# Kernel tuning notes

Measured on AMD Instinct MI355X. Metric: run time of the kernel, lower is better.

The kernel has to match this reference:

```python
import jax, jax.numpy as jnp
import numpy as np

N = 30000      # nodes
E = 480000     # edges (before self loops)
NFEAT = 128
H = 16         # heads
C = 32         # per-head channels = nhid
NCLASS = 10
G = 64         # graphs in batch
ATT_SLOPE = 0.2   # GATv2Conv negative_slope default
ACT_SLOPE = 0.01  # F.leaky_relu default


def setup_inputs() -> dict:
    key = jax.random.key(0)
    ks = jax.random.split(key, 16)
    def glorot(k, shape):
        fan = sum(shape[:2]) if len(shape) > 1 else shape[0]
        return jax.random.normal(k, shape, jnp.float32) * (2.0 / fan) ** 0.5
    inp = {
        "x": jax.random.normal(ks[0], (N, NFEAT), jnp.float32),
        # layer 1: lin_l / lin_r map NFEAT -> H*C, attention vector att [H, C]
        "Wl1": glorot(ks[1], (NFEAT, H * C)), "bl1": jnp.zeros((H * C,), jnp.float32),
        "Wr1": glorot(ks[2], (NFEAT, H * C)), "br1": jnp.zeros((H * C,), jnp.float32),
        "att1": glorot(ks[3], (H, C)), "b1": jnp.zeros((C,), jnp.float32),
        # layer 2: nhid(=C) -> H*C
        "Wl2": glorot(ks[4], (C, H * C)), "bl2": jnp.zeros((H * C,), jnp.float32),
        "Wr2": glorot(ks[5], (C, H * C)), "br2": jnp.zeros((H * C,), jnp.float32),
        "att2": glorot(ks[6], (H, C)), "b2": jnp.zeros((C,), jnp.float32),
        # classifier nhid -> nclass
        "Wc": glorot(ks[7], (C, NCLASS)), "bc": jnp.zeros((NCLASS,), jnp.float32),
        "edge_index": jax.random.randint(ks[8], (2, E), 0, N, jnp.int32),
        "batch": jnp.sort(jax.random.randint(ks[9], (N,), 0, G, jnp.int32)),
    }
    return inp


def _gatv2_layer(x, Wl, bl, Wr, br, att, b, src, dst, n):
    # GATv2Conv, concat=False (mean over heads), eval mode (no dropout)
    xl = (x @ Wl + bl).reshape(n, H, C)   # messages (x_j)
    xr = (x @ Wr + br).reshape(n, H, C)   # query side (x_i)
    e = jax.nn.leaky_relu(xl[src] + xr[dst], ATT_SLOPE)      # [E', H, C]
    score = jnp.einsum('ehc,hc->eh', e, att)                 # [E', H]
    # segment softmax over incoming edges of each dst node
    m = jax.ops.segment_max(score, dst, num_segments=n)
    ex = jnp.exp(score - m[dst])
    denom = jax.ops.segment_sum(ex, dst, num_segments=n)
    alpha = ex / denom[dst]                                  # [E', H]
    out = jax.ops.segment_sum(alpha[:, :, None] * xl[src], dst, num_segments=n)
    return out.mean(axis=1) + b                              # [n, C]


def reference(x, Wl1, bl1, Wr1, br1, att1, b1, Wl2, bl2, Wr2, br2, att2, b2, Wc, bc, edge_index, batch):
    # add self loops (PyG GATv2Conv default add_self_loops=True)
    loop = jnp.arange(N, dtype=edge_index.dtype)
    src = jnp.concatenate([edge_index[0], loop])
    dst = jnp.concatenate([edge_index[1], loop])

    h = jax.nn.leaky_relu(_gatv2_layer(x, Wl1, bl1, Wr1, br1, att1, b1, src, dst, N), ACT_SLOPE)
    h = jax.nn.leaky_relu(_gatv2_layer(h, Wl2, bl2, Wr2, br2, att2, b2, src, dst, N), ACT_SLOPE)
    # dropout is identity in eval mode
    # global mean pool over graphs
    summed = jax.ops.segment_sum(h, batch, num_segments=G)               # [G, C]
    counts = jax.ops.segment_sum(jnp.ones((N,), h.dtype), batch, num_segments=G)
    pooled = summed / jnp.maximum(counts, 1.0)[:, None]
    logits = pooled @ Wc + bc
    return logits / 1.0  # temperature = 1.0
```

## Files before the change

kernel.cpp:

```cpp
#include <hip/hip_runtime.h>
#include <float.h>

#define NNODES 30000
#define NEDGES 480000
#define NFEATK 128
#define NH 16
#define NC 32
#define HC 512
#define NCLASSES 10
#define NG 64
#define CAP 96

using half2v = __attribute__((ext_vector_type(2))) _Float16;
using half4 = __attribute__((ext_vector_type(4))) _Float16;
using half8 = __attribute__((ext_vector_type(8))) _Float16;
using f32x4 = __attribute__((ext_vector_type(4))) float;

__global__ void prep0_kernel(const float* __restrict__ Wl1, const float* __restrict__ Wr1,
                             _Float16* __restrict__ Wlt1, _Float16* __restrict__ Wrt1,
                             const float* __restrict__ Wl2, const float* __restrict__ Wr2,
                             _Float16* __restrict__ Wlt2, _Float16* __restrict__ Wrt2,
                             int* __restrict__ cnt, unsigned short* __restrict__ csr) {
    int gtid = blockIdx.x * blockDim.x + threadIdx.x;
    int gstride = gridDim.x * blockDim.x;
    for (int i = gtid; i < 2 * 512 * NFEATK; i += gstride) {
        int sel = i >= 512 * NFEATK;
        int idx = i - sel * 512 * NFEATK;
        const float* W = sel ? Wr1 : Wl1;
        _Float16* Wt = sel ? Wrt1 : Wlt1;
        int n = idx & 511, k = idx >> 9;
        Wt[n * NFEATK + k] = (_Float16)W[idx];
    }
    for (int i = gtid; i < 2 * 512 * NC; i += gstride) {
        int sel = i >= 512 * NC;
        int idx = i - sel * 512 * NC;
        const float* W = sel ? Wr2 : Wl2;
        _Float16* Wt = sel ? Wrt2 : Wlt2;
        int n = idx & 511, k = idx >> 9;
        Wt[n * NC + k] = (_Float16)W[idx];
    }
    for (int i = gtid; i < NNODES; i += gstride) {
        cnt[i] = 1;
        csr[i * CAP] = (unsigned short)i;
    }
}

__global__ void scatter_kernel(const int* __restrict__ src, const int* __restrict__ dst,
                               int* __restrict__ cnt, unsigned short* __restrict__ csr) {
    int e = blockIdx.x * blockDim.x + threadIdx.x;
    if (e >= NEDGES) return;
    int s = src[e], d = dst[e];
    int pos = atomicAdd(&cnt[d], 1);
    csr[d * CAP + pos] = (unsigned short)s;
}

template <int K, typename AT>
__launch_bounds__(256)
__global__ void dual_gemm_kernel(const AT* __restrict__ A,
                                 const _Float16* __restrict__ Wlt, const _Float16* __restrict__ Wrt,
                                 const float* __restrict__ bl, const float* __restrict__ br,
                                 _Float16* __restrict__ Yl, _Float16* __restrict__ Yr) {
    constexpr int KS = (K > 64) ? 64 : K;
    constexpr int KcS = KS / 8;
    constexpr int AH = 64 * KS;
    constexpr int BH = 128 * KS;
    constexpr int YSH = 64 * 136;
    constexpr int SMEMH = (AH + 2 * BH > YSH) ? (AH + 2 * BH) : YSH;
    __shared__ __align__(16) _Float16 smem[SMEMH];
    _Float16* as = smem;
    _Float16* bsl = smem + AH;
    _Float16* bsr = smem + AH + BH;

    int tid = threadIdx.x;
    int nbase = blockIdx.x * 128;
    int mb = blockIdx.y;

    int wave = tid >> 6, lane = tid & 63;
    int quad = lane >> 4, l16 = lane & 15;
    int am = l16 & (KcS - 1);

    f32x4 accl[8], accr[8];
    #pragma unroll
    for (int f = 0; f < 8; f++) {
        accl[f] = (f32x4){0.f, 0.f, 0.f, 0.f};
        accr[f] = (f32x4){0.f, 0.f, 0.f, 0.f};
    }

    #pragma unroll
    for (int ko = 0; ko < K / KS; ++ko) {
        if (ko) __syncthreads();
        for (int c = tid; c < 64 * KcS; c += 256) {
            int row = c / KcS, k8 = c % KcS;
            int arow = mb * 64 + row; if (arow > NNODES - 1) arow = NNODES - 1;
            half8 v;
            if constexpr (sizeof(AT) == 4) {
                const float* ap = (const float*)&A[(size_t)arow * K + (ko * KcS + k8) * 8];
                float4 f0 = *(const float4*)ap;
                float4 f1 = *(const float4*)(ap + 4);
                v = half8{(_Float16)f0.x, (_Float16)f0.y, (_Float16)f0.z, (_Float16)f0.w,
                          (_Float16)f1.x, (_Float16)f1.y, (_Float16)f1.z, (_Float16)f1.w};
            } else {
                v = *(const half8*)&A[(size_t)arow * K + (ko * KcS + k8) * 8];
            }
            *(half8*)&as[(row * KcS + (k8 ^ (row & (KcS - 1)))) * 8] = v;
        }
        for (int c = tid; c < 2 * 128 * KcS; c += 256) {
            int sel = c >= 128 * KcS;
            int cc = c - sel * 128 * KcS;
            int row = cc / KcS, k8 = cc % KcS;
            const _Float16* Bt = sel ? Wrt : Wlt;
            _Float16* bs = sel ? bsr : bsl;
            half8 v = *(const half8*)&Bt[(size_t)(nbase + row) * K + (ko * KcS + k8) * 8];
            *(half8*)&bs[(row * KcS + (k8 ^ (row & (KcS - 1)))) * 8] = v;
        }
        __syncthreads();

        #pragma unroll
        for (int kk = 0; kk < KcS; kk += 4) {
            int k8 = (kk + quad) ^ am;
            half8 a = *(const half8*)&as[((wave * 16 + l16) * KcS + k8) * 8];
            #pragma unroll
            for (int f = 0; f < 8; f++) {
                half8 b = *(const half8*)&bsl[((f * 16 + l16) * KcS + k8) * 8];
                accl[f] = __builtin_amdgcn_mfma_f32_16x16x32_f16(a, b, accl[f], 0, 0, 0);
            }
            #pragma unroll
            for (int f = 0; f < 8; f++) {
                half8 b = *(const half8*)&bsr[((f * 16 + l16) * KcS + k8) * 8];
                accr[f] = __builtin_amdgcn_mfma_f32_16x16x32_f16(a, b, accr[f], 0, 0, 0);
            }
        }
    }
    __syncthreads();

    _Float16* ys = smem;
    int mtop = mb * 64;
    #pragma unroll
    for (int f = 0; f < 8; f++) {
        float bv = bl[nbase + f * 16 + l16];
        #pragma unroll
        for (int r = 0; r < 4; r++)
            ys[(wave * 16 + quad * 4 + r) * 136 + f * 16 + l16] = (_Float16)(accl[f][r] + bv);
    }
    __syncthreads();
    for (int c = tid; c < 64 * 16; c += 256) {
        int r = c >> 4, cc = (c & 15) * 8;
        int grow = mtop + r;
        if (grow < NNODES)
            *(half8*)&Yl[(size_t)grow * HC + nbase + cc] = *(half8*)&ys[r * 136 + cc];
    }
    __syncthreads();
    #pragma unroll
    for (int f = 0; f < 8; f++) {
        float bv = br[nbase + f * 16 + l16];
        #pragma unroll
        for (int r = 0; r < 4; r++)
            ys[(wave * 16 + quad * 4 + r) * 136 + f * 16 + l16] = (_Float16)(accr[f][r] + bv);
    }
    __syncthreads();
    for (int c = tid; c < 64 * 16; c += 256) {
        int r = c >> 4, cc = (c & 15) * 8;
        int grow = mtop + r;
        if (grow < NNODES)
            *(half8*)&Yr[(size_t)grow * HC + nbase + cc] = *(half8*)&ys[r * 136 + cc];
    }
}

__device__ inline half2v lrelu2(half2v e) {
    half2v s = e * half2v{(_Float16)0.2f, (_Float16)0.2f};
    return __builtin_elementwise_max(e, s);
}

#if __has_builtin(__builtin_amdgcn_fdot2)
#define FDOT2(a, b, c) __builtin_amdgcn_fdot2((a), (b), (c), false)
#else
__device__ inline float fdot2_sw(half2v a, half2v b, float c) {
    half2v p = a * b;
    return c + (float)p.x + (float)p.y;
}
#define FDOT2(a, b, c) fdot2_sw((a), (b), (c))
#endif

template <typename OUT>
__launch_bounds__(256)
__global__ void gat_edge_kernel(const _Float16* __restrict__ xlh, const _Float16* __restrict__ xrh,
                                const float* __restrict__ att, const float* __restrict__ bvec,
                                const int* __restrict__ cnt, const unsigned short* __restrict__ csr_src,
                                OUT* __restrict__ hout) {
    int wv = threadIdx.x >> 6;
    int t = threadIdx.x & 63;
    int d = blockIdx.x * 4 + wv;
    int col = t * 8;

    half8 xrq = *(const half8*)&xrh[(unsigned)d * HC + col];
    half2v xr0 = {xrq[0], xrq[1]}, xr1 = {xrq[2], xrq[3]};
    half2v xr2 = {xrq[4], xrq[5]}, xr3 = {xrq[6], xrq[7]};
    float4 atta = *(const float4*)&att[col];
    float4 attb = *(const float4*)&att[col + 4];
    half2v at0 = {(_Float16)atta.x, (_Float16)atta.y};
    half2v at1 = {(_Float16)atta.z, (_Float16)atta.w};
    half2v at2 = {(_Float16)attb.x, (_Float16)attb.y};
    half2v at3 = {(_Float16)attb.z, (_Float16)attb.w};

    int beg = d * CAP, end = beg + cnt[d];

    float l = 0.f;
    float a[8];
    #pragma unroll
    for (int c = 0; c < 8; c++) a[c] = 0.f;

    for (int i = beg; i < end; i += 8) {
        int n = end - i;
        int sx[8];
        #pragma unroll
        for (int j = 0; j < 8; j++) sx[j] = csr_src[i + (j < n ? j : 0)];
        half8 q[8];
        #pragma unroll
        for (int j = 0; j < 8; j++) q[j] = *(const half8*)&xlh[(unsigned)sx[j] * HC + col];

        float v[8];
        #pragma unroll
        for (int j = 0; j < 8; j++) {
            float vv = 0.f;
            vv = FDOT2(lrelu2(half2v{q[j][0], q[j][1]} + xr0), at0, vv);
            vv = FDOT2(lrelu2(half2v{q[j][2], q[j][3]} + xr1), at1, vv);
            vv = FDOT2(lrelu2(half2v{q[j][4], q[j][5]} + xr2), at2, vv);
            vv = FDOT2(lrelu2(half2v{q[j][6], q[j][7]} + xr3), at3, vv);
            vv += __shfl_xor(vv, 1);
            vv += __shfl_xor(vv, 2);
            v[j] = vv;
        }
        #pragma unroll
        for (int j = 0; j < 8; j++) {
            float p = (j < n) ? __expf(v[j]) : 0.f;
            l += p;
            #pragma unroll
            for (int c = 0; c < 8; c++) a[c] += p * (float)q[j][c];
        }
    }

    float inv = 1.0f / l;
    #pragma unroll
    for (int c = 0; c < 8; c++) a[c] *= inv;

    #pragma unroll
    for (int off = 4; off < 64; off <<= 1) {
        #pragma unroll
        for (int c = 0; c < 8; c++) a[c] += __shfl_xor(a[c], off);
    }

    if (t < 4) {
        #pragma unroll
        for (int c = 0; c < 8; c++) {
            float r = a[c] * (1.0f / (float)NH) + bvec[t * 8 + c];
            r = (r > 0.f) ? r : 0.01f * r;
            hout[(size_t)d * NC + t * 8 + c] = (OUT)r;
        }
    }
}

__launch_bounds__(1024)
__global__ void pool_classify_kernel(const float* __restrict__ h, const int* __restrict__ batch,
                                     const float* __restrict__ Wc, const float* __restrict__ bc,
                                     float* __restrict__ out) {
    int g = blockIdx.x;
    int lo = 0, hi = NNODES;
    while (lo < hi) { int mid = (lo + hi) >> 1; if (batch[mid] < g) lo = mid + 1; else hi = mid; }
    int start = lo;
    hi = NNODES;
    while (lo < hi) { int mid = (lo + hi) >> 1; if (batch[mid] <= g) lo = mid + 1; else hi = mid; }
    int endn = lo;
    int cntg = endn - start;

    int tid = threadIdx.x;
    int c = tid & 31, nl = tid >> 5;
    float s = 0.f;
    for (int n = start + nl; n < endn; n += 32) s += h[n * NC + c];
    __shared__ float red[1024];
    red[tid] = s;
    __syncthreads();
    if (tid < 32) {
        float t = 0.f;
        #pragma unroll
        for (int j = 0; j < 32; j++) t += red[j * 32 + tid];
        red[tid] = t / fmaxf((float)cntg, 1.0f);
    }
    __syncthreads();
    if (tid < NCLASSES) {
        float sum = bc[tid];
        #pragma unroll
        for (int cc = 0; cc < NC; cc++) sum += red[cc] * Wc[cc * NCLASSES + tid];
        out[g * NCLASSES + tid] = sum;
    }
}


extern "C" void kernel_launch(void* const* d_in, const int* in_sizes, int n_in,
                              void* d_out, int out_size, void* d_ws, size_t ws_size,
                              hipStream_t stream) {
    const float* x    = (const float*)d_in[0];
    const float* Wl1  = (const float*)d_in[1];
    const float* bl1  = (const float*)d_in[2];
    const float* Wr1  = (const float*)d_in[3];
    const float* br1  = (const float*)d_in[4];
    const float* att1 = (const float*)d_in[5];
    const float* b1   = (const float*)d_in[6];
    const float* Wl2  = (const float*)d_in[7];
    const float* bl2  = (const float*)d_in[8];
    const float* Wr2  = (const float*)d_in[9];
    const float* br2  = (const float*)d_in[10];
    const float* att2 = (const float*)d_in[11];
    const float* b2   = (const float*)d_in[12];
    const float* Wc   = (const float*)d_in[13];
    const float* bc   = (const float*)d_in[14];
    const int* ei     = (const int*)d_in[15];
    const int* batch  = (const int*)d_in[16];
    float* out = (float*)d_out;

    const int* srcp = ei;
    const int* dstp = ei + NEDGES;

    char* ws = (char*)d_ws;
    size_t off = 0;
    auto alloc = [&](size_t bytes) -> void* {
        void* p = ws + off;
        off += (bytes + 255) & ~(size_t)255;
        return p;
    };
    _Float16* xlh  = (_Float16*)alloc(sizeof(_Float16) * (size_t)NNODES * HC);
    _Float16* xrh  = (_Float16*)alloc(sizeof(_Float16) * (size_t)NNODES * HC);
    _Float16* h1   = (_Float16*)alloc(sizeof(_Float16) * (size_t)NNODES * NC);
    float* h2      = (float*)alloc(sizeof(float) * (size_t)NNODES * NC);
    _Float16* Wlt1 = (_Float16*)alloc(sizeof(_Float16) * 512 * NFEATK);
    _Float16* Wrt1 = (_Float16*)alloc(sizeof(_Float16) * 512 * NFEATK);
    _Float16* Wlt2 = (_Float16*)alloc(sizeof(_Float16) * 512 * NC);
    _Float16* Wrt2 = (_Float16*)alloc(sizeof(_Float16) * 512 * NC);
    int*   cnt     = (int*)alloc(sizeof(int) * NNODES);
    unsigned short* csr = (unsigned short*)alloc(sizeof(unsigned short) * (size_t)NNODES * CAP);

    prep0_kernel<<<256, 256, 0, stream>>>(Wl1, Wr1, Wlt1, Wrt1,
                                          Wl2, Wr2, Wlt2, Wrt2, cnt, csr);
    scatter_kernel<<<(NEDGES + 255) / 256, 256, 0, stream>>>(srcp, dstp, cnt, csr);

    const int MB = (NNODES + 63) / 64;

    dual_gemm_kernel<NFEATK, float><<<dim3(4, MB), 256, 0, stream>>>(x, Wlt1, Wrt1, bl1, br1, xlh, xrh);
    gat_edge_kernel<_Float16><<<NNODES / 4, 256, 0, stream>>>(xlh, xrh, att1, b1, cnt, csr, h1);

    dual_gemm_kernel<NC, _Float16><<<dim3(4, MB), 256, 0, stream>>>(h1, Wlt2, Wrt2, bl2, br2, xlh, xrh);
    gat_edge_kernel<float><<<NNODES / 4, 256, 0, stream>>>(xlh, xrh, att2, b2, cnt, csr, h2);

    pool_classify_kernel<<<NG, 1024, 0, stream>>>(h2, batch, Wc, bc, out);
}
```

Baseline: 357.3 us.

## Fuse prep and edge scatter into one kernel; shrink gather batch to 4 edges

Merges the weight-transpose prep and the CSR scatter into a single kernel. Self loops are now inserted by atomics like ordinary edges, after a memset of the counts. Separately, the edge-attention loop now processes 4 neighbours per iteration instead of 8, which cuts register pressure and wasted padded gathers at the cost of less memory-level parallelism per thread. Self loops are no longer guaranteed to sit first in each row, so the summation order changes.

Measured after the change: 340.1 us. 1.05x faster.

```diff
diff --git a/kernel.cpp b/kernel.cpp
--- a/kernel.cpp
+++ b/kernel.cpp
@@ -16,13 +16,21 @@
 using half8 = __attribute__((ext_vector_type(8))) _Float16;
 using f32x4 = __attribute__((ext_vector_type(4))) float;
 
-__global__ void prep0_kernel(const float* __restrict__ Wl1, const float* __restrict__ Wr1,
-                             _Float16* __restrict__ Wlt1, _Float16* __restrict__ Wrt1,
-                             const float* __restrict__ Wl2, const float* __restrict__ Wr2,
-                             _Float16* __restrict__ Wlt2, _Float16* __restrict__ Wrt2,
-                             int* __restrict__ cnt, unsigned short* __restrict__ csr) {
+__global__ void prep_scatter_kernel(const int* __restrict__ src, const int* __restrict__ dst,
+                                    int* __restrict__ cnt, unsigned short* __restrict__ csr,
+                                    const float* __restrict__ Wl1, const float* __restrict__ Wr1,
+                                    _Float16* __restrict__ Wlt1, _Float16* __restrict__ Wrt1,
+                                    const float* __restrict__ Wl2, const float* __restrict__ Wr2,
+                                    _Float16* __restrict__ Wlt2, _Float16* __restrict__ Wrt2) {
     int gtid = blockIdx.x * blockDim.x + threadIdx.x;
     int gstride = gridDim.x * blockDim.x;
+    for (int i = gtid; i < NEDGES + NNODES; i += gstride) {
+        int s, d;
+        if (i < NEDGES) { s = src[i]; d = dst[i]; }
+        else            { d = i - NEDGES; s = d; }
+        int pos = atomicAdd(&cnt[d], 1);
+        csr[d * CAP + pos] = (unsigned short)s;
+    }
     for (int i = gtid; i < 2 * 512 * NFEATK; i += gstride) {
         int sel = i >= 512 * NFEATK;
         int idx = i - sel * 512 * NFEATK;
@@ -39,19 +47,6 @@
         int n = idx & 511, k = idx >> 9;
         Wt[n * NC + k] = (_Float16)W[idx];
     }
-    for (int i = gtid; i < NNODES; i += gstride) {
-        cnt[i] = 1;
-        csr[i * CAP] = (unsigned short)i;
-    }
-}
-
-__global__ void scatter_kernel(const int* __restrict__ src, const int* __restrict__ dst,
-                               int* __restrict__ cnt, unsigned short* __restrict__ csr) {
-    int e = blockIdx.x * blockDim.x + threadIdx.x;
-    if (e >= NEDGES) return;
-    int s = src[e], d = dst[e];
-    int pos = atomicAdd(&cnt[d], 1);
-    csr[d * CAP + pos] = (unsigned short)s;
 }
 
 template <int K, typename AT>
@@ -209,33 +204,52 @@
     #pragma unroll
     for (int c = 0; c < 8; c++) a[c] = 0.f;
 
-    for (int i = beg; i < end; i += 8) {
+    for (int i = beg; i < end; i += 4) {
         int n = end - i;
-        int sx[8];
-        #pragma unroll
-        for (int j = 0; j < 8; j++) sx[j] = csr_src[i + (j < n ? j : 0)];
-        half8 q[8];
-        #pragma unroll
-        for (int j = 0; j < 8; j++) q[j] = *(const half8*)&xlh[(unsigned)sx[j] * HC + col];
-
-        float v[8];
-        #pragma unroll
-        for (int j = 0; j < 8; j++) {
-            float vv = 0.f;
-            vv = FDOT2(lrelu2(half2v{q[j][0], q[j][1]} + xr0), at0, vv);
-            vv = FDOT2(lrelu2(half2v{q[j][2], q[j][3]} + xr1), at1, vv);
-            vv = FDOT2(lrelu2(half2v{q[j][4], q[j][5]} + xr2), at2, vv);
-            vv = FDOT2(lrelu2(half2v{q[j][6], q[j][7]} + xr3), at3, vv);
-            vv += __shfl_xor(vv, 1);
-            vv += __shfl_xor(vv, 2);
-            v[j] = vv;
-        }
-        #pragma unroll
-        for (int j = 0; j < 8; j++) {
-            float p = (j < n) ? __expf(v[j]) : 0.f;
-            l += p;
-            #pragma unroll
-            for (int c = 0; c < 8; c++) a[c] += p * (float)q[j][c];
+        int s0 = csr_src[i];
+        int s1 = csr_src[n > 1 ? i + 1 : i];
+        int s2 = csr_src[n > 2 ? i + 2 : i];
+        int s3 = csr_src[n > 3 ? i + 3 : i];
+        half8 q0 = *(const half8*)&xlh[(unsigned)s0 * HC + col];
+        half8 q1 = *(const half8*)&xlh[(unsigned)s1 * HC + col];
+        half8 q2 = *(const half8*)&xlh[(unsigned)s2 * HC + col];
+        half8 q3 = *(const half8*)&xlh[(unsigned)s3 * HC + col];
+
+        float v0 = 0.f, v1 = 0.f, v2 = 0.f, v3 = 0.f;
+        v0 = FDOT2(lrelu2(half2v{q0[0], q0[1]} + xr0), at0, v0);
+        v0 = FDOT2(lrelu2(half2v{q0[2], q0[3]} + xr1), at1, v0);
+        v0 = FDOT2(lrelu2(half2v{q0[4], q0[5]} + xr2), at2, v0);
+        v0 = FDOT2(lrelu2(half2v{q0[6], q0[7]} + xr3), at3, v0);
+        v1 = FDOT2(lrelu2(half2v{q1[0], q1[1]} + xr0), at0, v1);
+        v1 = FDOT2(lrelu2(half2v{q1[2], q1[3]} + xr1), at1, v1);
+        v1 = FDOT2(lrelu2(half2v{q1[4], q1[5]} + xr2), at2, v1);
+        v1 = FDOT2(lrelu2(half2v{q1[6], q1[7]} + xr3), at3, v1);
+        v2 = FDOT2(lrelu2(half2v{q2[0], q2[1]} + xr0), at0, v2);
+        v2 = FDOT2(lrelu2(half2v{q2[2], q2[3]} + xr1), at1, v2);
+        v2 = FDOT2(lrelu2(half2v{q2[4], q2[5]} + xr2), at2, v2);
+        v2 = FDOT2(lrelu2(half2v{q2[6], q2[7]} + xr3), at3, v2);
+        v3 = FDOT2(lrelu2(half2v{q3[0], q3[1]} + xr0), at0, v3);
+        v3 = FDOT2(lrelu2(half2v{q3[2], q3[3]} + xr1), at1, v3);
+        v3 = FDOT2(lrelu2(half2v{q3[4], q3[5]} + xr2), at2, v3);
+        v3 = FDOT2(lrelu2(half2v{q3[6], q3[7]} + xr3), at3, v3);
+
+        v0 += __shfl_xor(v0, 1); v1 += __shfl_xor(v1, 1);
+        v2 += __shfl_xor(v2, 1); v3 += __shfl_xor(v3, 1);
+        v0 += __shfl_xor(v0, 2); v1 += __shfl_xor(v1, 2);
+        v2 += __shfl_xor(v2, 2); v3 += __shfl_xor(v3, 2);
+
+        float p0 = __expf(v0);
+        float p1 = (n > 1) ? __expf(v1) : 0.f;
+        float p2 = (n > 2) ? __expf(v2) : 0.f;
+        float p3 = (n > 3) ? __expf(v3) : 0.f;
+        l += (p0 + p1) + (p2 + p3);
+
+        #pragma unroll
+        for (int c = 0; c < 8; c++) {
+            a[c] += p0 * (float)q0[c];
+            a[c] += p1 * (float)q1[c];
+            a[c] += p2 * (float)q2[c];
+            a[c] += p3 * (float)q3[c];
         }
     }
 
@@ -338,9 +352,10 @@
     int*   cnt     = (int*)alloc(sizeof(int) * NNODES);
     unsigned short* csr = (unsigned short*)alloc(sizeof(unsigned short) * (size_t)NNODES * CAP);
 
-    prep0_kernel<<<256, 256, 0, stream>>>(Wl1, Wr1, Wlt1, Wrt1,
-                                          Wl2, Wr2, Wlt2, Wrt2, cnt, csr);
-    scatter_kernel<<<(NEDGES + 255) / 256, 256, 0, stream>>>(srcp, dstp, cnt, csr);
+    hipMemsetAsync(cnt, 0, sizeof(int) * NNODES, stream);
+
+    prep_scatter_kernel<<<(NEDGES + NNODES + 255) / 256, 256, 0, stream>>>(
+        srcp, dstp, cnt, csr, Wl1, Wr1, Wlt1, Wrt1, Wl2, Wr2, Wlt2, Wrt2);
 
     const int MB = (NNODES + 63) / 64;
 
```
